# Optimization experiments

Measured on AMD Instinct MI355X. Metric: run time of the kernel, lower is better.

Reference implementation:

```python
import jax, jax.numpy as jnp
import numpy as np

N = 20000          # nodes
E = 320000         # edges
G = 256            # g_dim
H1 = 256           # h1_dim (RGCN out)
H2 = 128           # h2_dim (per-head transformer out)
HEADS = 4
R = 8              # num relations
EPS_BN = 1e-5


def setup_inputs() -> dict:
    key = jax.random.key(0)
    ks = jax.random.split(key, 16)
    inp = {
        "node_features": jax.random.normal(ks[0], (N, G), jnp.float32),
        "node_type": jax.random.randint(ks[1], (N,), 0, 3),
        "edge_index": jax.random.randint(ks[2], (2, E), 0, N),
        "edge_type": jax.random.randint(ks[3], (E,), 0, R),
        # RGCNConv params
        "W_rel": jax.random.normal(ks[4], (R, G, H1), jnp.float32) * (1.0 / np.sqrt(G)),
        "W_root": jax.random.normal(ks[5], (G, H1), jnp.float32) * (1.0 / np.sqrt(G)),
        "b_rgcn": jnp.zeros((H1,), jnp.float32),
        # TransformerConv params (concat=True -> HEADS*H2 output)
        "W_q": jax.random.normal(ks[6], (H1, HEADS * H2), jnp.float32) * (1.0 / np.sqrt(H1)),
        "b_q": jnp.zeros((HEADS * H2,), jnp.float32),
        "W_k": jax.random.normal(ks[7], (H1, HEADS * H2), jnp.float32) * (1.0 / np.sqrt(H1)),
        "b_k": jnp.zeros((HEADS * H2,), jnp.float32),
        "W_v": jax.random.normal(ks[8], (H1, HEADS * H2), jnp.float32) * (1.0 / np.sqrt(H1)),
        "b_v": jnp.zeros((HEADS * H2,), jnp.float32),
        "W_skip": jax.random.normal(ks[9], (H1, HEADS * H2), jnp.float32) * (1.0 / np.sqrt(H1)),
        "b_skip": jnp.zeros((HEADS * H2,), jnp.float32),
        # BatchNorm1d params (training-mode batch stats)
        "bn_gamma": jnp.ones((HEADS * H2,), jnp.float32),
        "bn_beta": jnp.zeros((HEADS * H2,), jnp.float32),
    }
    return inp


def reference(node_features, node_type, edge_index, edge_type,
              W_rel, W_root, b_rgcn,
              W_q, b_q, W_k, b_k, W_v, b_v, W_skip, b_skip,
              bn_gamma, bn_beta):
    x = node_features
    src, dst = edge_index[0], edge_index[1]  # messages flow src -> dst

    # ---- RGCNConv (mean aggregation per relation, root weight, bias) ----
    xr = jnp.einsum('nd,rdh->nrh', x, W_rel)           # (N, R, H1)
    msg = xr[src, edge_type]                            # (E, H1)
    seg = dst * R + edge_type                           # combined (node, relation) segment id
    sums = jax.ops.segment_sum(msg, seg, num_segments=N * R)
    cnt = jax.ops.segment_sum(jnp.ones((E,), x.dtype), seg, num_segments=N * R)
    mean = sums / jnp.maximum(cnt, 1.0)[:, None]
    agg = mean.reshape(N, R, H1).sum(axis=1)            # sum over relations
    h1 = agg + x @ W_root + b_rgcn                      # (N, H1)

    # ---- TransformerConv (heads=HEADS, concat=True, root skip) ----
    q = (h1 @ W_q + b_q).reshape(N, HEADS, H2)
    k = (h1 @ W_k + b_k).reshape(N, HEADS, H2)
    v = (h1 @ W_v + b_v).reshape(N, HEADS, H2)

    scale = 1.0 / np.sqrt(H2)
    alpha = jnp.sum(q[dst] * k[src], axis=-1) * scale   # (E, HEADS)
    amax = jax.ops.segment_max(alpha, dst, num_segments=N)  # per-dst softmax max
    ea = jnp.exp(alpha - amax[dst])
    denom = jax.ops.segment_sum(ea, dst, num_segments=N)
    attn = ea / jnp.maximum(denom[dst], 1e-16)          # (E, HEADS)

    out = jax.ops.segment_sum(attn[:, :, None] * v[src], dst, num_segments=N)
    out = out.reshape(N, HEADS * H2) + h1 @ W_skip + b_skip

    # ---- BatchNorm1d (batch stats) + LeakyReLU(0.01) ----
    mu = out.mean(axis=0)
    var = out.var(axis=0)
    xn = (out - mu) * jax.lax.rsqrt(var + EPS_BN)
    y = bn_gamma * xn + bn_beta
    return jax.nn.leaky_relu(y, negative_slope=0.01)
```

## Files before the change

### kernel.cpp

```cpp
#include <hip/hip_runtime.h>

static const int N_NODES = 20000;
static const int N_EDGES = 320000;
static const int GDIM    = 256;
static const int H1DIM   = 256;
static const int C2DIM   = 512;
static const int NREL    = 8;
static const int NSEG    = N_NODES * NREL;

typedef _Float16 __attribute__((ext_vector_type(8))) half8;
typedef _Float16 __attribute__((ext_vector_type(4))) half4;
typedef __attribute__((ext_vector_type(4))) float f32x4;

__device__ __forceinline__ void gload_lds16(const void* g, void* l) {
  __builtin_amdgcn_global_load_lds(
      (const __attribute__((address_space(1))) unsigned int*)g,
      (__attribute__((address_space(3))) unsigned int*)l, 16, 0, 0);
}

__device__ __forceinline__ void swz_bxy(int& bx, int& by) {
  int nx   = gridDim.x;
  int nwg  = nx * gridDim.y;
  int orig = blockIdx.y * nx + blockIdx.x;
  int xcd  = orig & 7;
  int q    = nwg >> 3, r = nwg & 7;
  int base = xcd < r ? xcd * (q + 1) : r * (q + 1) + (xcd - r) * q;
  int wgid = base + (orig >> 3);
  bx = wgid % nx; by = wgid / nx;
}

template<int OUT_HALF>
__global__ __launch_bounds__(256) void gemm_mfma_k(
    const _Float16* __restrict__ A, const _Float16* __restrict__ Bt,
    const float* __restrict__ bias, void* __restrict__ Cout,
    int M, int N, int K)
{
  __shared__ _Float16 As[128 * 64];
  __shared__ _Float16 Bs[128 * 64];
  int bx, by; swz_bxy(bx, by);
  const int tid  = threadIdx.x;
  const int wid  = tid >> 6, lane = tid & 63;
  const int wr   = wid >> 1, wc = wid & 1;
  const int brow = by * 128;
  const int bcol = bx * 128;
  const int l15  = lane & 15, lhi = lane >> 4;
  const int srow = wid * 32;
  const int lrow = lane >> 3;
  const int lchk = lane & 7;

  f32x4 acc[4][4] = {};

  for (int k0 = 0; k0 < K; k0 += 64) {
    __syncthreads();
#pragma unroll
    for (int i = 0; i < 4; ++i) {
      int row = srow + i * 8 + lrow;
      int gc  = lchk ^ (row & 7);
      gload_lds16(A  + (size_t)(brow + row) * K + k0 + gc * 8,
                  &As[(srow + i * 8) * 64]);
      gload_lds16(Bt + (size_t)(bcol + row) * K + k0 + gc * 8,
                  &Bs[(srow + i * 8) * 64]);
    }
    __syncthreads();
#pragma unroll
    for (int kf = 0; kf < 2; ++kf) {
      int cc = kf * 4 + lhi;
      half8 af[4], bfr[4];
#pragma unroll
      for (int mi = 0; mi < 4; ++mi) {
        int row = wr * 64 + mi * 16 + l15;
        af[mi] = ((const half8*)As)[row * 8 + (cc ^ (row & 7))];
      }
#pragma unroll
      for (int ni = 0; ni < 4; ++ni) {
        int row = wc * 64 + ni * 16 + l15;
        bfr[ni] = ((const half8*)Bs)[row * 8 + (cc ^ (row & 7))];
      }
#pragma unroll
      for (int mi = 0; mi < 4; ++mi)
#pragma unroll
        for (int ni = 0; ni < 4; ++ni)
          acc[mi][ni] = __builtin_amdgcn_mfma_f32_16x16x32_f16(
              af[mi], bfr[ni], acc[mi][ni], 0, 0, 0);
    }
  }
#pragma unroll
  for (int ni = 0; ni < 4; ++ni) {
    int col = bcol + wc * 64 + ni * 16 + l15;
    float bb = bias ? bias[col] : 0.f;
#pragma unroll
    for (int mi = 0; mi < 4; ++mi) {
      int row0 = brow + wr * 64 + mi * 16 + lhi * 4;
#pragma unroll
      for (int j = 0; j < 4; ++j) {
        int r = row0 + j;
        if (r >= M) continue;
        float val = acc[mi][ni][j] + bb;
        if (OUT_HALF) ((_Float16*)Cout)[(size_t)r * N + col] = (_Float16)val;
        else          ((float*)Cout)[(size_t)r * N + col] = val;
      }
    }
  }
}

__global__ __launch_bounds__(256) void prep_k(
    const int* __restrict__ dst, const int* __restrict__ et, int* __restrict__ hist,
    const float* __restrict__ W_root, const float* __restrict__ W_rel,
    _Float16* __restrict__ Wt_cat,
    const float* __restrict__ Wq, const float* __restrict__ Wk,
    const float* __restrict__ Wv, const float* __restrict__ Ws,
    const float* __restrict__ bq, const float* __restrict__ bk,
    const float* __restrict__ bv, const float* __restrict__ bs,
    _Float16* __restrict__ Wt_qk, float* __restrict__ bias_cat,
    const float* __restrict__ x, _Float16* __restrict__ xh)
{
  int b = blockIdx.x, tid = threadIdx.x;
  if (b < 1250) {
    int e = b * 256 + tid;
    if (e < N_EDGES) atomicAdd(&hist[dst[e] * NREL + et[e]], 1);
  } else if (b < 3554) {
    int idx = (b - 1250) * 256 + tid;
    int k = idx % 2304, n = idx / 2304;
    float v = (k < 256) ? W_root[(size_t)k * H1DIM + n]
                        : W_rel[(size_t)(k - 256) * H1DIM + n];
    Wt_cat[(size_t)n * 2304 + k] = (_Float16)v;
  } else if (b < 5602) {
    int idx = (b - 3554) * 256 + tid;
    int n = idx >> 8, k = idx & 255;
    int sel = n >> 9, c = n & 511;
    const float* W = sel == 0 ? Wq : sel == 1 ? Wk : sel == 2 ? Wv : Ws;
    Wt_qk[(size_t)n * 256 + k] = (_Float16)W[(size_t)k * C2DIM + c];
    if (k == 0) {
      const float* B = sel == 0 ? bq : sel == 1 ? bk : sel == 2 ? bv : bs;
      bias_cat[n] = B[c];
    }
  } else {
    int i = (b - 5602) * 256 + tid;
    float4 v = ((const float4*)x)[i];
    half4 o = {(_Float16)v.x, (_Float16)v.y, (_Float16)v.z, (_Float16)v.w};
    ((half4*)xh)[i] = o;
  }
}

__global__ __launch_bounds__(1024) void scan_local_k(
    const int* __restrict__ in, int* __restrict__ out, int* __restrict__ bsum, int n)
{
  __shared__ int s[1024];
  int gi = blockIdx.x * 1024 + threadIdx.x;
  int v = gi < n ? in[gi] : 0;
  s[threadIdx.x] = v; __syncthreads();
  for (int off = 1; off < 1024; off <<= 1) {
    int t = threadIdx.x >= off ? s[threadIdx.x - off] : 0;
    __syncthreads();
    s[threadIdx.x] += t;
    __syncthreads();
  }
  if (gi < n) out[gi] = s[threadIdx.x] - v;
  if (threadIdx.x == 1023) bsum[blockIdx.x] = s[1023];
}

__global__ __launch_bounds__(1024) void scan_small_k(int* __restrict__ bsum, int nb)
{
  __shared__ int s[1024];
  int v = threadIdx.x < nb ? bsum[threadIdx.x] : 0;
  s[threadIdx.x] = v; __syncthreads();
  for (int off = 1; off < 1024; off <<= 1) {
    int t = threadIdx.x >= off ? s[threadIdx.x - off] : 0;
    __syncthreads();
    s[threadIdx.x] += t;
    __syncthreads();
  }
  if (threadIdx.x < nb) bsum[threadIdx.x] = s[threadIdx.x] - v;
}

__global__ void scan_addoff_k(int* __restrict__ off, const int* __restrict__ bsum,
                              int* __restrict__ cur, int n)
{
  int gi = blockIdx.x * 1024 + threadIdx.x;
  if (gi < n) {
    int v = off[gi] + bsum[blockIdx.x];
    off[gi] = v;
    cur[gi] = v;
  }
  if (gi == 0) off[n] = N_EDGES;
}

__global__ void reorder_k(const int* __restrict__ src, const int* __restrict__ dst,
                          const int* __restrict__ et,
                          int* __restrict__ cur, int* __restrict__ esrc)
{
  int e = blockIdx.x * blockDim.x + threadIdx.x;
  if (e >= N_EDGES) return;
  int seg = dst[e] * NREL + et[e];
  esrc[atomicAdd(&cur[seg], 1)] = src[e];
}

__global__ __launch_bounds__(256) void agg_xcat_k(
    const _Float16* __restrict__ xh, const int* __restrict__ off,
    const int* __restrict__ esrc, _Float16* __restrict__ Xcat)
{
  int d = blockIdx.x * 4 + (threadIdx.x >> 6);
  if (d >= N_NODES) return;
  int lane = threadIdx.x & 63;
  _Float16* xrow = Xcat + (size_t)d * 2304;
  half4 xv = ((const half4*)(xh + (size_t)d * GDIM))[lane];
  *(half4*)(xrow + lane * 4) = xv;
  for (int r = 0; r < NREL; ++r) {
    int seg = d * NREL + r;
    int beg = off[seg], end = off[seg + 1];
    float4 acc = make_float4(0.f, 0.f, 0.f, 0.f);
    for (int e = beg; e < end; ++e) {
      int s = esrc[e];
      half4 v = ((const half4*)(xh + (size_t)s * GDIM))[lane];
      acc.x += (float)v.x; acc.y += (float)v.y;
      acc.z += (float)v.z; acc.w += (float)v.w;
    }
    float inv = (end > beg) ? 1.0f / (float)(end - beg) : 0.0f;
    half4 o;
    o.x = (_Float16)(acc.x * inv); o.y = (_Float16)(acc.y * inv);
    o.z = (_Float16)(acc.z * inv); o.w = (_Float16)(acc.w * inv);
    *(half4*)(xrow + 256 + r * 256 + lane * 4) = o;
  }
}

__global__ __launch_bounds__(256) void attn_fused_k(
    const _Float16* __restrict__ qkvs,
    const int* __restrict__ off, const int* __restrict__ esrc,
    float* __restrict__ out)
{
  int d = blockIdx.x * 4 + (threadIdx.x >> 6);
  if (d >= N_NODES) return;
  int lane = threadIdx.x & 63;
  half8 qr = ((const half8*)(qkvs + (size_t)d * 2048))[lane];
  float qf[8];
#pragma unroll
  for (int j = 0; j < 8; ++j) qf[j] = (float)qr[j];
  float m = -3.4e38f, ssum = 0.f;
  float av[8] = {};
  int beg = off[d * NREL], end = off[d * NREL + NREL];
  half8 krN = {}, vrN = {};
  if (beg < end) {
    int s0 = esrc[beg];
    const half8* row = (const half8*)(qkvs + (size_t)s0 * 2048 + 512);
    krN = row[lane];
    vrN = row[64 + lane];
  }
  for (int e = beg; e < end; ++e) {
    half8 kr = krN, vr = vrN;
    if (e + 1 < end) {
      int s1 = esrc[e + 1];
      const half8* row = (const half8*)(qkvs + (size_t)s1 * 2048 + 512);
      krN = row[lane];
      vrN = row[64 + lane];
    }
    float p = 0.f;
#pragma unroll
    for (int j = 0; j < 8; ++j) p += qf[j] * (float)kr[j];
    p += __shfl_xor(p, 1); p += __shfl_xor(p, 2);
    p += __shfl_xor(p, 4); p += __shfl_xor(p, 8);
    float a = p * 0.08838834764831845f;
    float mn = fmaxf(m, a);
    float corr = __expf(m - mn), w = __expf(a - mn);
    ssum = ssum * corr + w;
#pragma unroll
    for (int j = 0; j < 8; ++j) av[j] = av[j] * corr + w * (float)vr[j];
    m = mn;
  }
  float inv = 1.0f / fmaxf(ssum, 1e-16f);
  half8 sr = ((const half8*)(qkvs + (size_t)d * 2048 + 1536))[lane];
  float* orow = out + (size_t)d * C2DIM + lane * 8;
#pragma unroll
  for (int j = 0; j < 8; ++j) orow[j] = av[j] * inv + (float)sr[j];
}

__global__ __launch_bounds__(512) void bn_stats_k(
    const float* __restrict__ x, float* __restrict__ sums, float* __restrict__ sumsq)
{
  int c = threadIdx.x;
  float s = 0.f, sq = 0.f;
  for (int row = blockIdx.x; row < N_NODES; row += gridDim.x) {
    float v = x[(size_t)row * C2DIM + c];
    s += v; sq += v * v;
  }
  atomicAdd(&sums[c], s);
  atomicAdd(&sumsq[c], sq);
}

__global__ void bn_apply_k(float* __restrict__ x,
                           const float* __restrict__ sums, const float* __restrict__ sumsq,
                           const float* __restrict__ gamma, const float* __restrict__ beta,
                           int total4)
{
  int i = blockIdx.x * blockDim.x + threadIdx.x;
  if (i >= total4) return;
  int c0 = (i & 127) * 4;
  float4 v = ((const float4*)x)[i];
  float o[4] = {v.x, v.y, v.z, v.w};
#pragma unroll
  for (int j = 0; j < 4; ++j) {
    int c = c0 + j;
    float mu  = sums[c] * (1.0f / N_NODES);
    float var = sumsq[c] * (1.0f / N_NODES) - mu * mu;
    float sc  = gamma[c] * rsqrtf(var + 1e-5f);
    float val = (o[j] - mu) * sc + beta[c];
    o[j] = val >= 0.f ? val : 0.01f * val;
  }
  ((float4*)x)[i] = make_float4(o[0], o[1], o[2], o[3]);
}

extern "C" void kernel_launch(void* const* d_in, const int* in_sizes, int n_in,
                              void* d_out, int out_size, void* d_ws, size_t ws_size,
                              hipStream_t stream)
{
  const float* x      = (const float*)d_in[0];
  const int*   ei     = (const int*)d_in[2];
  const int*   src    = ei;
  const int*   dst    = ei + N_EDGES;
  const int*   etype  = (const int*)d_in[3];
  const float* W_rel  = (const float*)d_in[4];
  const float* W_root = (const float*)d_in[5];
  const float* b_rgcn = (const float*)d_in[6];
  const float* W_q = (const float*)d_in[7];  const float* b_q = (const float*)d_in[8];
  const float* W_k = (const float*)d_in[9];  const float* b_k = (const float*)d_in[10];
  const float* W_v = (const float*)d_in[11]; const float* b_v = (const float*)d_in[12];
  const float* W_s = (const float*)d_in[13]; const float* b_s = (const float*)d_in[14];
  const float* gamma = (const float*)d_in[15];
  const float* beta  = (const float*)d_in[16];
  float* out = (float*)d_out;

  char* ws = (char*)d_ws;
  _Float16* Xcat   = (_Float16*)(ws + 0);
  _Float16* QKVS   = (_Float16*)(ws + 0);
  _Float16* Wt_cat = (_Float16*)(ws + 92160000);
  _Float16* Wt_qk  = (_Float16*)(ws + 93339648);
  _Float16* h1h    = (_Float16*)(ws + 94388224);
  _Float16* xh     = h1h;

  char* C = ws + 104628224;
  int*   cur      = (int*)(C + 0);
  float* bns      = (float*)(C + 640000);
  float* bias_cat = (float*)(C + 648192);
  int*   off      = (int*)(C + 656384);
  int*   esrc     = (int*)(C + 1296400);
  int*   bsum     = (int*)(C + 2576400);
  float* bnsum = bns, *bnsq = bns + 512;

  hipMemsetAsync(C, 0, 648192, stream);

  dim3 blk(256);
  const int NB = (NSEG + 1023) / 1024;

  prep_k<<<dim3(10602), blk, 0, stream>>>(
      dst, etype, cur,
      W_root, W_rel, Wt_cat,
      W_q, W_k, W_v, W_s, b_q, b_k, b_v, b_s, Wt_qk, bias_cat,
      x, xh);

  scan_local_k<<<dim3(NB), dim3(1024), 0, stream>>>(cur, off, bsum, NSEG);
  scan_small_k<<<dim3(1), dim3(1024), 0, stream>>>(bsum, NB);
  scan_addoff_k<<<dim3(NB), dim3(1024), 0, stream>>>(off, bsum, cur, NSEG);
  reorder_k<<<dim3((N_EDGES + 255) / 256), blk, 0, stream>>>(
      src, dst, etype, cur, esrc);

  agg_xcat_k<<<dim3((N_NODES + 3) / 4), blk, 0, stream>>>(xh, off, esrc, Xcat);

  gemm_mfma_k<1><<<dim3(H1DIM / 128, (N_NODES + 127) / 128), blk, 0, stream>>>(
      Xcat, Wt_cat, b_rgcn, h1h, N_NODES, H1DIM, 2304);

  gemm_mfma_k<1><<<dim3(2048 / 128, (N_NODES + 127) / 128), blk, 0, stream>>>(
      h1h, Wt_qk, bias_cat, QKVS, N_NODES, 2048, 256);

  attn_fused_k<<<dim3((N_NODES + 3) / 4), blk, 0, stream>>>(QKVS, off, esrc, out);

  bn_stats_k<<<dim3(208), dim3(512), 0, stream>>>(out, bnsum, bnsq);
  bn_apply_k<<<dim3((N_NODES * C2DIM / 4 + 255) / 256), blk, 0, stream>>>(
      out, bnsum, bnsq, gamma, beta, N_NODES * C2DIM / 4);
}
```

Baseline: 357.6 us.

## Transform-then-aggregate RGCN, fp16 attention output, merge scan kernels

Reorders the RGCN so that one GEMM first projects x through the root and all relation weights (N x 2304 output, K=256). A gather kernel then averages the projected rows per relation and adds the root term and bias, replacing the old gather into a 2304-wide concatenated input followed by a K=2304 GEMM. The attention output is stored as fp16 so the batch-norm stats and apply passes read half the bytes. The small block-sum scan is folded into the offset-add kernel, which removes one launch. In exchange the gather now reads 256-wide fp16 rows out of a much larger intermediate, and there is extra rounding from storing the pre-BN activations in fp16.

```diff
diff --git a/kernel.cpp b/kernel.cpp
--- a/kernel.cpp
+++ b/kernel.cpp
@@ -10,6 +10,7 @@
 
 typedef _Float16 __attribute__((ext_vector_type(8))) half8;
 typedef _Float16 __attribute__((ext_vector_type(4))) half4;
+typedef _Float16 __attribute__((ext_vector_type(2))) half2v;
 typedef __attribute__((ext_vector_type(4))) float f32x4;
 
 __device__ __forceinline__ void gload_lds16(const void* g, void* l) {
@@ -106,7 +107,7 @@
 __global__ __launch_bounds__(256) void prep_k(
     const int* __restrict__ dst, const int* __restrict__ et, int* __restrict__ hist,
     const float* __restrict__ W_root, const float* __restrict__ W_rel,
-    _Float16* __restrict__ Wt_cat,
+    _Float16* __restrict__ Wt_cat2,
     const float* __restrict__ Wq, const float* __restrict__ Wk,
     const float* __restrict__ Wv, const float* __restrict__ Ws,
     const float* __restrict__ bq, const float* __restrict__ bk,
@@ -120,10 +121,14 @@
     if (e < N_EDGES) atomicAdd(&hist[dst[e] * NREL + et[e]], 1);
   } else if (b < 3554) {
     int idx = (b - 1250) * 256 + tid;
-    int k = idx % 2304, n = idx / 2304;
-    float v = (k < 256) ? W_root[(size_t)k * H1DIM + n]
-                        : W_rel[(size_t)(k - 256) * H1DIM + n];
-    Wt_cat[(size_t)n * 2304 + k] = (_Float16)v;
+    int n2 = idx >> 8, k = idx & 255;
+    float v;
+    if (n2 < 256) v = W_root[(size_t)k * H1DIM + n2];
+    else {
+      int rr = (n2 - 256) >> 8, c = (n2 - 256) & 255;
+      v = W_rel[((size_t)rr * 256 + k) * 256 + c];
+    }
+    Wt_cat2[idx] = (_Float16)v;
   } else if (b < 5602) {
     int idx = (b - 3554) * 256 + tid;
     int n = idx >> 8, k = idx & 255;
@@ -159,28 +164,26 @@
   if (threadIdx.x == 1023) bsum[blockIdx.x] = s[1023];
 }
 
-__global__ __launch_bounds__(1024) void scan_small_k(int* __restrict__ bsum, int nb)
+__global__ __launch_bounds__(1024) void scan_addoff_k(
+    int* __restrict__ off, const int* __restrict__ bsum,
+    int* __restrict__ cur, int n, int nb)
 {
   __shared__ int s[1024];
-  int v = threadIdx.x < nb ? bsum[threadIdx.x] : 0;
-  s[threadIdx.x] = v; __syncthreads();
-  for (int off = 1; off < 1024; off <<= 1) {
-    int t = threadIdx.x >= off ? s[threadIdx.x - off] : 0;
-    __syncthreads();
-    s[threadIdx.x] += t;
-    __syncthreads();
-  }
-  if (threadIdx.x < nb) bsum[threadIdx.x] = s[threadIdx.x] - v;
-}
-
-__global__ void scan_addoff_k(int* __restrict__ off, const int* __restrict__ bsum,
-                              int* __restrict__ cur, int n)
-{
-  int gi = blockIdx.x * 1024 + threadIdx.x;
+  int t = threadIdx.x;
+  int v = t < nb ? bsum[t] : 0;
+  s[t] = v; __syncthreads();
+  for (int o = 1; o < 1024; o <<= 1) {
+    int u = t >= o ? s[t - o] : 0;
+    __syncthreads();
+    s[t] += u;
+    __syncthreads();
+  }
+  int blockOff = blockIdx.x == 0 ? 0 : s[blockIdx.x - 1];
+  int gi = blockIdx.x * 1024 + t;
   if (gi < n) {
-    int v = off[gi] + bsum[blockIdx.x];
-    off[gi] = v;
-    cur[gi] = v;
+    int val = off[gi] + blockOff;
+    off[gi] = val;
+    cur[gi] = val;
   }
   if (gi == 0) off[n] = N_EDGES;
 }
@@ -195,38 +198,41 @@
   esrc[atomicAdd(&cur[seg], 1)] = src[e];
 }
 
-__global__ __launch_bounds__(256) void agg_xcat_k(
-    const _Float16* __restrict__ xh, const int* __restrict__ off,
-    const int* __restrict__ esrc, _Float16* __restrict__ Xcat)
+__global__ __launch_bounds__(256) void agg_h1_k(
+    const _Float16* __restrict__ Y, const float* __restrict__ b_rgcn,
+    const int* __restrict__ off, const int* __restrict__ esrc,
+    _Float16* __restrict__ h1h)
 {
   int d = blockIdx.x * 4 + (threadIdx.x >> 6);
   if (d >= N_NODES) return;
   int lane = threadIdx.x & 63;
-  _Float16* xrow = Xcat + (size_t)d * 2304;
-  half4 xv = ((const half4*)(xh + (size_t)d * GDIM))[lane];
-  *(half4*)(xrow + lane * 4) = xv;
+  half4 rt = ((const half4*)(Y + (size_t)d * 2304))[lane];
+  float4 bb = ((const float4*)b_rgcn)[lane];
+  float4 acc = make_float4((float)rt.x + bb.x, (float)rt.y + bb.y,
+                           (float)rt.z + bb.z, (float)rt.w + bb.w);
   for (int r = 0; r < NREL; ++r) {
     int seg = d * NREL + r;
     int beg = off[seg], end = off[seg + 1];
-    float4 acc = make_float4(0.f, 0.f, 0.f, 0.f);
+    if (beg >= end) continue;
+    float4 a2 = make_float4(0.f, 0.f, 0.f, 0.f);
     for (int e = beg; e < end; ++e) {
       int s = esrc[e];
-      half4 v = ((const half4*)(xh + (size_t)s * GDIM))[lane];
-      acc.x += (float)v.x; acc.y += (float)v.y;
-      acc.z += (float)v.z; acc.w += (float)v.w;
-    }
-    float inv = (end > beg) ? 1.0f / (float)(end - beg) : 0.0f;
-    half4 o;
-    o.x = (_Float16)(acc.x * inv); o.y = (_Float16)(acc.y * inv);
-    o.z = (_Float16)(acc.z * inv); o.w = (_Float16)(acc.w * inv);
-    *(half4*)(xrow + 256 + r * 256 + lane * 4) = o;
-  }
+      half4 v = ((const half4*)(Y + (size_t)s * 2304 + 256 + r * 256))[lane];
+      a2.x += (float)v.x; a2.y += (float)v.y;
+      a2.z += (float)v.z; a2.w += (float)v.w;
+    }
+    float inv = 1.0f / (float)(end - beg);
+    acc.x += a2.x * inv; acc.y += a2.y * inv;
+    acc.z += a2.z * inv; acc.w += a2.w * inv;
+  }
+  half4 o = {(_Float16)acc.x, (_Float16)acc.y, (_Float16)acc.z, (_Float16)acc.w};
+  ((half4*)(h1h + (size_t)d * 256))[lane] = o;
 }
 
 __global__ __launch_bounds__(256) void attn_fused_k(
     const _Float16* __restrict__ qkvs,
     const int* __restrict__ off, const int* __restrict__ esrc,
-    float* __restrict__ out)
+    _Float16* __restrict__ outh)
 {
   int d = blockIdx.x * 4 + (threadIdx.x >> 6);
   if (d >= N_NODES) return;
@@ -268,44 +274,47 @@
   }
   float inv = 1.0f / fmaxf(ssum, 1e-16f);
   half8 sr = ((const half8*)(qkvs + (size_t)d * 2048 + 1536))[lane];
-  float* orow = out + (size_t)d * C2DIM + lane * 8;
-#pragma unroll
-  for (int j = 0; j < 8; ++j) orow[j] = av[j] * inv + (float)sr[j];
-}
-
-__global__ __launch_bounds__(512) void bn_stats_k(
-    const float* __restrict__ x, float* __restrict__ sums, float* __restrict__ sumsq)
-{
-  int c = threadIdx.x;
-  float s = 0.f, sq = 0.f;
+  half8 o;
+#pragma unroll
+  for (int j = 0; j < 8; ++j) o[j] = (_Float16)(av[j] * inv + (float)sr[j]);
+  ((half8*)(outh + (size_t)d * C2DIM))[lane] = o;
+}
+
+__global__ __launch_bounds__(256) void bn_stats_k(
+    const _Float16* __restrict__ x, float* __restrict__ sums, float* __restrict__ sumsq)
+{
+  int t = threadIdx.x;
+  float s0 = 0.f, q0 = 0.f, s1 = 0.f, q1 = 0.f;
   for (int row = blockIdx.x; row < N_NODES; row += gridDim.x) {
-    float v = x[(size_t)row * C2DIM + c];
-    s += v; sq += v * v;
-  }
-  atomicAdd(&sums[c], s);
-  atomicAdd(&sumsq[c], sq);
-}
-
-__global__ void bn_apply_k(float* __restrict__ x,
+    half2v v = ((const half2v*)(x + (size_t)row * C2DIM))[t];
+    float a = (float)v.x, b = (float)v.y;
+    s0 += a; q0 += a * a; s1 += b; q1 += b * b;
+  }
+  atomicAdd(&sums[2 * t], s0);  atomicAdd(&sums[2 * t + 1], s1);
+  atomicAdd(&sumsq[2 * t], q0); atomicAdd(&sumsq[2 * t + 1], q1);
+}
+
+__global__ void bn_apply_k(const _Float16* __restrict__ xin, float* __restrict__ xout,
                            const float* __restrict__ sums, const float* __restrict__ sumsq,
                            const float* __restrict__ gamma, const float* __restrict__ beta,
-                           int total4)
+                           int total8)
 {
   int i = blockIdx.x * blockDim.x + threadIdx.x;
-  if (i >= total4) return;
-  int c0 = (i & 127) * 4;
-  float4 v = ((const float4*)x)[i];
-  float o[4] = {v.x, v.y, v.z, v.w};
-#pragma unroll
-  for (int j = 0; j < 4; ++j) {
+  if (i >= total8) return;
+  int c0 = (i & 63) * 8;
+  half8 v = ((const half8*)xin)[i];
+  float o[8];
+#pragma unroll
+  for (int j = 0; j < 8; ++j) {
     int c = c0 + j;
     float mu  = sums[c] * (1.0f / N_NODES);
     float var = sumsq[c] * (1.0f / N_NODES) - mu * mu;
     float sc  = gamma[c] * rsqrtf(var + 1e-5f);
-    float val = (o[j] - mu) * sc + beta[c];
+    float val = ((float)v[j] - mu) * sc + beta[c];
     o[j] = val >= 0.f ? val : 0.01f * val;
   }
-  ((float4*)x)[i] = make_float4(o[0], o[1], o[2], o[3]);
+  ((float4*)xout)[i * 2]     = make_float4(o[0], o[1], o[2], o[3]);
+  ((float4*)xout)[i * 2 + 1] = make_float4(o[4], o[5], o[6], o[7]);
 }
 
 extern "C" void kernel_launch(void* const* d_in, const int* in_sizes, int n_in,
@@ -329,8 +338,9 @@
   float* out = (float*)d_out;
 
   char* ws = (char*)d_ws;
-  _Float16* Xcat   = (_Float16*)(ws + 0);
+  _Float16* Y      = (_Float16*)(ws + 0);
   _Float16* QKVS   = (_Float16*)(ws + 0);
+  _Float16* outh   = (_Float16*)(ws + 81920000);
   _Float16* Wt_cat = (_Float16*)(ws + 92160000);
   _Float16* Wt_qk  = (_Float16*)(ws + 93339648);
   _Float16* h1h    = (_Float16*)(ws + 94388224);
@@ -357,22 +367,21 @@
       x, xh);
 
   scan_local_k<<<dim3(NB), dim3(1024), 0, stream>>>(cur, off, bsum, NSEG);
-  scan_small_k<<<dim3(1), dim3(1024), 0, stream>>>(bsum, NB);
-  scan_addoff_k<<<dim3(NB), dim3(1024), 0, stream>>>(off, bsum, cur, NSEG);
+  scan_addoff_k<<<dim3(NB), dim3(1024), 0, stream>>>(off, bsum, cur, NSEG, NB);
   reorder_k<<<dim3((N_EDGES + 255) / 256), blk, 0, stream>>>(
       src, dst, etype, cur, esrc);
 
-  agg_xcat_k<<<dim3((N_NODES + 3) / 4), blk, 0, stream>>>(xh, off, esrc, Xcat);
-
-  gemm_mfma_k<1><<<dim3(H1DIM / 128, (N_NODES + 127) / 128), blk, 0, stream>>>(
-      Xcat, Wt_cat, b_rgcn, h1h, N_NODES, H1DIM, 2304);
+  gemm_mfma_k<1><<<dim3(2304 / 128, (N_NODES + 127) / 128), blk, 0, stream>>>(
+      xh, Wt_cat, nullptr, Y, N_NODES, 2304, 256);
+
+  agg_h1_k<<<dim3((N_NODES + 3) / 4), blk, 0, stream>>>(Y, b_rgcn, off, esrc, h1h);
 
   gemm_mfma_k<1><<<dim3(2048 / 128, (N_NODES + 127) / 128), blk, 0, stream>>>(
       h1h, Wt_qk, bias_cat, QKVS, N_NODES, 2048, 256);
 
-  attn_fused_k<<<dim3((N_NODES + 3) / 4), blk, 0, stream>>>(QKVS, off, esrc, out);
-
-  bn_stats_k<<<dim3(208), dim3(512), 0, stream>>>(out, bnsum, bnsq);
-  bn_apply_k<<<dim3((N_NODES * C2DIM / 4 + 255) / 256), blk, 0, stream>>>(
-      out, bnsum, bnsq, gamma, beta, N_NODES * C2DIM / 4);
-}
+  attn_fused_k<<<dim3((N_NODES + 3) / 4), blk, 0, stream>>>(QKVS, off, esrc, outh);
+
+  bn_stats_k<<<dim3(208), blk, 0, stream>>>(outh, bnsum, bnsq);
+  bn_apply_k<<<dim3((N_NODES * C2DIM / 8 + 255) / 256), blk, 0, stream>>>(
+      outh, out, bnsum, bnsq, gamma, beta, N_NODES * C2DIM / 8);
+}
```

Measured after the change: 369.7 us. +3.4%, slower.
